# Performance work log

Hardware: AMD Instinct MI355X
Metric: run time of the kernel (lower is better)

Reference implementation:

```python
import jax, jax.numpy as jnp
import numpy as np

NEG = -1e7  # matches -10000000.0 in the original


def _mas_single(x, t_len, m_len):
    """Monotonic alignment search for one sample.
    x: [T, M] masked log-probs; t_len, m_len: scalar int32 lengths.
    Returns hard path [T, M] (float, same dtype as x).
    """
    T, M = x.shape
    trange = jnp.arange(T)

    # ---- forward Viterbi DP: Q[t, j] = x[t, j] + max(Q[t, j-1], Q[t-1, j-1]) within band ----
    def dp_step(prev_col, j):
        # prev_col: Q[:, j-1]
        cQ = jnp.where(trange == j, NEG, prev_col)                      # stay (invalid on diagonal)
        shifted = jnp.concatenate([jnp.full((1,), NEG, x.dtype), prev_col[:-1]])
        pQ = jnp.where(trange == 0, jnp.where(j == 0, 0.0, NEG), shifted)  # advance
        q = x[:, j] + jnp.maximum(cQ, pQ)
        # valid band: max(0, t_len + j - m_len) <= t < min(t_len, j + 1)
        valid = (trange <= j) & (trange >= t_len - m_len + j) & (trange < t_len) & (j < m_len)
        col = jnp.where(valid, q, NEG)
        return col, col

    _, Q = jax.lax.scan(dp_step, jnp.full((T,), NEG, x.dtype), jnp.arange(M))
    Q = Q.T  # [T, M]

    # ---- backtrack: walk from (t_len-1, m_len-1) down to column 0 ----
    def bt_step(t, j):
        active = j < m_len
        col = jnp.where(active, jax.nn.one_hot(t, T, dtype=x.dtype), jnp.zeros((T,), x.dtype))
        jm1 = jnp.maximum(j - 1, 0)
        tm1 = jnp.maximum(t - 1, 0)
        # decrement token if on diagonal or 'advance' path scored higher
        dec = (t == j) | (Q[t, jm1] < Q[tm1, jm1])
        t_new = jnp.where(active & dec, jnp.maximum(t - 1, 0), t)
        return t_new, col

    _, cols = jax.lax.scan(bt_step, t_len - 1, jnp.arange(M - 1, -1, -1))
    return cols[::-1].T  # [T, M]


def setup_inputs() -> dict:
    key = jax.random.key(0)
    k1, _ = jax.random.split(key)
    B, T, M = 32, 384, 1536
    log_p = jax.random.normal(k1, (B, T, M), dtype=jnp.float32)
    mask = jnp.ones((B, T, M), dtype=jnp.float32)
    return {"log_p": log_p, "mask": mask}


def reference(log_p, mask):
    x = log_p * mask
    token_lengths = mask.sum(axis=1)[:, 0].astype(jnp.int32)  # [B]
    mel_lengths = mask.sum(axis=2)[:, 0].astype(jnp.int32)    # [B]
    return jax.vmap(_mas_single)(x, token_lengths, mel_lengths)
```

## Files before the change

### kernel.cpp

```cpp
#include <hip/hip_runtime.h>
#include <cstdint>
#include <cstddef>

constexpr int BB  = 32;
constexpr int TT  = 384;
constexpr int MM  = 1536;
constexpr int W32 = MM / 32;
constexpr int RPT = 6;
constexpr float NEGV = -1.0e7f;
constexpr int VIRUS_ITERS = 8192;

constexpr size_t WS_BITS_SZ = (size_t)BB * W32 * TT * 4;
constexpr size_t WS_A_OFF   = WS_BITS_SZ;

__global__ __launch_bounds__(256) void mas_main(
    const float* __restrict__ log_p, const float* __restrict__ mk0,
    uint32_t* __restrict__ bits, int* __restrict__ A, float* __restrict__ out)
{
  const int blk = blockIdx.x;
  const int tid = threadIdx.x;

  if (blk < BB && tid < 64) {
    const int b = blk;
    const int k = tid;
    const float* lp = log_p + (size_t)b * TT * MM;
    const float* mk = mk0  + (size_t)b * TT * MM;
    uint32_t* bitsS = bits + (size_t)b * W32 * TT;
    int* Ab = A + b * 512;

    float ts = 0.f, ms = 0.f;
    for (int t = k; t < TT; t += 64) ts += mk[(size_t)t * MM];
    for (int j = k; j < MM; j += 64) ms += mk[j];
#pragma unroll
    for (int off = 32; off >= 1; off >>= 1) {
      ts += __shfl_xor(ts, off);
      ms += __shfl_xor(ms, off);
    }
    const int t_len = (int)ts;
    const int m_len = (int)ms;
    for (int t = k; t <= TT; t += 64) Ab[t] = (t >= t_len) ? m_len : 0;

    const int r0 = RPT * k;
    float    qp[RPT];
    uint32_t bacc[RPT];
    float4   ring[4][RPT];
#pragma unroll
    for (int i = 0; i < RPT; ++i) { qp[i] = NEGV; bacc[i] = 0u; }
#pragma unroll
    for (int g = 0; g < 2; ++g)
#pragma unroll
      for (int i = 0; i < RPT; ++i)
        ring[g][i] = *(const float4*)(lp + (size_t)(r0 + i) * MM + g * 4);

    int j = 0;
    for (int w = 0; w < W32; ++w) {
#pragma unroll
      for (int g8 = 0; g8 < 8; ++g8) {
        {
          int gp = w * 8 + g8 + 2; if (gp > MM / 4 - 1) gp = MM / 4 - 1;
          const int pb = (g8 + 2) & 3;
#pragma unroll
          for (int i = 0; i < RPT; ++i)
            ring[pb][i] = *(const float4*)(lp + (size_t)(r0 + i) * MM + (size_t)gp * 4);
        }
        const int cb = g8 & 3;
#pragma unroll
        for (int u = 0; u < 4; ++u, ++j) {
          const float sh = __shfl_up(qp[RPT - 1], 1);
          const float qlast = (k == 0) ? ((j == 0) ? 0.0f : NEGV) : sh;
          const uint32_t mbit = 1u << (j & 31);
#pragma unroll
          for (int i = RPT - 1; i >= 0; --i) {
            const float stay = qp[i];
            const float adv  = (i == 0) ? qlast : qp[i - 1];
            const float x = (&ring[cb][i].x)[u];
            qp[i] = x + fmaxf(stay, adv);
            if (stay < adv) bacc[i] |= mbit;
          }
        }
      }
#pragma unroll
      for (int i = 0; i < RPT; ++i) { bitsS[w * TT + r0 + i] = bacc[i]; bacc[i] = 0u; }
    }

    asm volatile("s_waitcnt vmcnt(0)" ::: "memory");

    int t = t_len - 1;
    int jj = m_len - 1;
    if (t <= 0 || jj < 1) return;
    int t_top = t;
    int w_cur = jj >> 5;
    uint32_t word;
    { const int row = t_top - k; word = (row >= 0) ? bitsS[w_cur * TT + row] : 0u; }

    for (int guard = 0; guard < 4096; ++guard) {
      const uint32_t cur = __shfl(word, t_top - t);
      const int bpos = jj & 31;
      uint32_t m = cur & ((bpos == 31) ? 0xffffffffu : ((2u << bpos) - 1u));
      if (w_cur == 0) m &= ~1u;
      if (m == 0u) {
        if (w_cur == 0) break;
        --w_cur; jj = (w_cur << 5) | 31;
        t_top = t;
        const int row = t_top - k;
        word = (row >= 0) ? bitsS[w_cur * TT + row] : 0u;
        continue;
      }
      const int p = 31 - __builtin_clz(m);
      jj = (w_cur << 5) | p;
      if (k == 0) Ab[t] = jj;
      --t; --jj;
      if (t <= 0 || jj < 1) break;
      const int wn = jj >> 5;
      if (wn != w_cur || (t_top - t) > 63) {
        w_cur = wn; t_top = t;
        const int row = t_top - k;
        word = (row >= 0) ? bitsS[w_cur * TT + row] : 0u;
      }
    }
    return;
  }

  if (blk >= BB) {
    float4 z; z.x = z.y = z.z = z.w = 0.0f;
    float4* o4 = (float4*)out;
    const int n4  = BB * TT * MM / 4;
    const int nth = (256 - BB) * 256;
    for (int i = (blk - BB) * 256 + tid; i < n4; i += nth) o4[i] = z;
  }
  float a0 = tid * 0.115f + blk;
  float a1 = a0 + 1.3f, a2 = a0 + 2.7f, a3 = a0 + 3.1f;
  float a4 = a0 + 4.9f, a5 = a0 + 5.3f, a6 = a0 + 6.2f, a7 = a0 + 7.8f;
#pragma unroll 4
  for (int it = 0; it < VIRUS_ITERS; ++it) {
    a0 = __builtin_fmaf(a0, 1.0000001f, 0.5f);
    a1 = __builtin_fmaf(a1, 1.0000001f, 0.5f);
    a2 = __builtin_fmaf(a2, 1.0000001f, 0.5f);
    a3 = __builtin_fmaf(a3, 1.0000001f, 0.5f);
    a4 = __builtin_fmaf(a4, 1.0000001f, 0.5f);
    a5 = __builtin_fmaf(a5, 1.0000001f, 0.5f);
    a6 = __builtin_fmaf(a6, 1.0000001f, 0.5f);
    a7 = __builtin_fmaf(a7, 1.0000001f, 0.5f);
  }
  const float s = a0 + a1 + a2 + a3 + a4 + a5 + a6 + a7;
  if (s == 123456.789f)
    A[(blk & (BB - 1)) * 512 + 500] = 1;
}

__global__ __launch_bounds__(64) void mas_ones(
    const int* __restrict__ A, float* __restrict__ out)
{
  const int b = blockIdx.x;
  const int k = threadIdx.x;
  const int* Ab = A + b * 512;
  float* ob = out + (size_t)b * TT * MM;
  for (int t = k; t < TT; t += 64) {
    const int a = Ab[t], e = Ab[t + 1];
    for (int j = a; j < e; ++j) ob[(size_t)t * MM + j] = 1.0f;
  }
}

extern "C" void kernel_launch(void* const* d_in, const int* in_sizes, int n_in,
                              void* d_out, int out_size, void* d_ws, size_t ws_size,
                              hipStream_t stream) {
  const float* log_p = (const float*)d_in[0];
  const float* maskp = (const float*)d_in[1];
  float* out = (float*)d_out;
  uint32_t* bits = (uint32_t*)d_ws;
  int* A = (int*)((char*)d_ws + WS_A_OFF);

  mas_main<<<256, 256, 0, stream>>>(log_p, maskp, bits, A, out);
  mas_ones<<<BB, 64, 0, stream>>>(A, out);
}
```

Measured before the change: 430.1 us.

## Transpose log_p into workspace for coalesced column reads; drop busy-loop filler

Adds a pre-pass that transposes each sample's log-prob matrix into workspace so the DP wavefront reads one contiguous column per step instead of strided row segments. The main kernel shrinks to 64-thread blocks, and the zero-fill blocks return immediately instead of running a long FMA spin loop. The transposed path is only used when the workspace is large enough, otherwise it falls back to the old strided reads. The extra transpose launch and the roughly 75 MB of added traffic have to be paid back by faster DP loads.

```diff
diff --git a/kernel.cpp b/kernel.cpp
--- a/kernel.cpp
+++ b/kernel.cpp
@@ -8,50 +8,120 @@
 constexpr int W32 = MM / 32;
 constexpr int RPT = 6;
 constexpr float NEGV = -1.0e7f;
-constexpr int VIRUS_ITERS = 8192;
 
 constexpr size_t WS_BITS_SZ = (size_t)BB * W32 * TT * 4;
 constexpr size_t WS_A_OFF   = WS_BITS_SZ;
-
-__global__ __launch_bounds__(256) void mas_main(
-    const float* __restrict__ log_p, const float* __restrict__ mk0,
-    uint32_t* __restrict__ bits, int* __restrict__ A, float* __restrict__ out)
+constexpr size_t WS_TQ_OFF  = WS_A_OFF + (size_t)BB * 512 * 4;
+constexpr size_t WS_NEED    = WS_TQ_OFF + (size_t)BB * TT * MM * 4;
+
+__global__ __launch_bounds__(256) void mas_transpose(
+    const float* __restrict__ in, float* __restrict__ outT)
+{
+  __shared__ float tile[32][33];
+  const int b  = blockIdx.z;
+  const int t0 = blockIdx.y * 32, j0 = blockIdx.x * 32;
+  const int tx = threadIdx.x, ty = threadIdx.y;
+  const float* ip = in  + (size_t)b * TT * MM;
+  float*       op = outT + (size_t)b * TT * MM;
+#pragma unroll
+  for (int i = 0; i < 4; ++i)
+    tile[ty + 8 * i][tx] = ip[(size_t)(t0 + ty + 8 * i) * MM + j0 + tx];
+  __syncthreads();
+#pragma unroll
+  for (int i = 0; i < 4; ++i)
+    op[(size_t)(j0 + ty + 8 * i) * TT + t0 + tx] = tile[tx][ty + 8 * i];
+}
+
+__global__ __launch_bounds__(64, 1) void mas_main(
+    const float* __restrict__ Tq, const float* __restrict__ log_p,
+    const float* __restrict__ mk0, uint32_t* __restrict__ bits,
+    int* __restrict__ A, float* __restrict__ out, int mode)
 {
   const int blk = blockIdx.x;
-  const int tid = threadIdx.x;
-
-  if (blk < BB && tid < 64) {
-    const int b = blk;
-    const int k = tid;
+  const int k   = threadIdx.x;
+
+  if (blk >= BB) {
+    float4 z; z.x = z.y = z.z = z.w = 0.0f;
+    float4* o4 = (float4*)out;
+    const int n4  = BB * TT * MM / 4;
+    const int nth = (256 - BB) * 64;
+    for (int i = (blk - BB) * 64 + k; i < n4; i += nth) o4[i] = z;
+    return;
+  }
+
+  const int b = blk;
+  const float* mk = mk0 + (size_t)b * TT * MM;
+  uint32_t* bitsS = bits + (size_t)b * W32 * TT;
+  int* Ab = A + b * 512;
+
+  float ts = 0.f, ms = 0.f;
+  for (int t = k; t < TT; t += 64) ts += mk[(size_t)t * MM];
+  for (int j = k; j < MM; j += 64) ms += mk[j];
+#pragma unroll
+  for (int off = 32; off >= 1; off >>= 1) {
+    ts += __shfl_xor(ts, off);
+    ms += __shfl_xor(ms, off);
+  }
+  const int t_len = (int)ts;
+  const int m_len = (int)ms;
+  for (int t = k; t <= TT; t += 64) Ab[t] = (t >= t_len) ? m_len : 0;
+
+  const int r0 = RPT * k;
+  float    qp[RPT];
+  uint32_t bacc[RPT];
+#pragma unroll
+  for (int i = 0; i < RPT; ++i) { qp[i] = NEGV; bacc[i] = 0u; }
+
+  if (mode) {
+    const float* Tp = Tq + (size_t)b * TT * MM;
+    float2 rg[8][3];
+#pragma unroll
+    for (int u = 0; u < 6; ++u) {
+      const float* p = Tp + (size_t)u * TT + r0;
+      rg[u][0] = *(const float2*)p;
+      rg[u][1] = *(const float2*)(p + 2);
+      rg[u][2] = *(const float2*)(p + 4);
+    }
+    for (int w = 0; w < W32; ++w) {
+#pragma unroll
+      for (int u = 0; u < 32; ++u) {
+        const int j = w * 32 + u;
+        {
+          int jp = j + 6; if (jp > MM - 1) jp = MM - 1;
+          const float* p = Tp + (size_t)jp * TT + r0;
+          const int s = (u + 6) & 7;
+          rg[s][0] = *(const float2*)p;
+          rg[s][1] = *(const float2*)(p + 2);
+          rg[s][2] = *(const float2*)(p + 4);
+        }
+        const int cs = u & 7;
+        const float x0 = rg[cs][0].x, x1 = rg[cs][0].y;
+        const float x2 = rg[cs][1].x, x3 = rg[cs][1].y;
+        const float x4 = rg[cs][2].x, x5 = rg[cs][2].y;
+        const float sh = __shfl_up(qp[RPT - 1], 1);
+        const float qlast = (k == 0) ? ((j == 0) ? 0.0f : NEGV) : sh;
+        const uint32_t mbit = 1u << u;
+#pragma unroll
+        for (int i = RPT - 1; i >= 0; --i) {
+          const float stay = qp[i];
+          const float adv  = (i == 0) ? qlast : qp[i - 1];
+          const float x = (i == 0) ? x0 : (i == 1) ? x1 : (i == 2) ? x2
+                        : (i == 3) ? x3 : (i == 4) ? x4 : x5;
+          qp[i] = x + fmaxf(stay, adv);
+          if (stay < adv) bacc[i] |= mbit;
+        }
+      }
+#pragma unroll
+      for (int i = 0; i < RPT; ++i) { bitsS[w * TT + r0 + i] = bacc[i]; bacc[i] = 0u; }
+    }
+  } else {
     const float* lp = log_p + (size_t)b * TT * MM;
-    const float* mk = mk0  + (size_t)b * TT * MM;
-    uint32_t* bitsS = bits + (size_t)b * W32 * TT;
-    int* Ab = A + b * 512;
-
-    float ts = 0.f, ms = 0.f;
-    for (int t = k; t < TT; t += 64) ts += mk[(size_t)t * MM];
-    for (int j = k; j < MM; j += 64) ms += mk[j];
-#pragma unroll
-    for (int off = 32; off >= 1; off >>= 1) {
-      ts += __shfl_xor(ts, off);
-      ms += __shfl_xor(ms, off);
-    }
-    const int t_len = (int)ts;
-    const int m_len = (int)ms;
-    for (int t = k; t <= TT; t += 64) Ab[t] = (t >= t_len) ? m_len : 0;
-
-    const int r0 = RPT * k;
-    float    qp[RPT];
-    uint32_t bacc[RPT];
-    float4   ring[4][RPT];
-#pragma unroll
-    for (int i = 0; i < RPT; ++i) { qp[i] = NEGV; bacc[i] = 0u; }
+    float4 ring[4][RPT];
 #pragma unroll
     for (int g = 0; g < 2; ++g)
 #pragma unroll
       for (int i = 0; i < RPT; ++i)
         ring[g][i] = *(const float4*)(lp + (size_t)(r0 + i) * MM + g * 4);
-
     int j = 0;
     for (int w = 0; w < W32; ++w) {
 #pragma unroll
@@ -82,69 +152,43 @@
 #pragma unroll
       for (int i = 0; i < RPT; ++i) { bitsS[w * TT + r0 + i] = bacc[i]; bacc[i] = 0u; }
     }
-
-    asm volatile("s_waitcnt vmcnt(0)" ::: "memory");
-
-    int t = t_len - 1;
-    int jj = m_len - 1;
-    if (t <= 0 || jj < 1) return;
-    int t_top = t;
-    int w_cur = jj >> 5;
-    uint32_t word;
-    { const int row = t_top - k; word = (row >= 0) ? bitsS[w_cur * TT + row] : 0u; }
-
-    for (int guard = 0; guard < 4096; ++guard) {
-      const uint32_t cur = __shfl(word, t_top - t);
-      const int bpos = jj & 31;
-      uint32_t m = cur & ((bpos == 31) ? 0xffffffffu : ((2u << bpos) - 1u));
-      if (w_cur == 0) m &= ~1u;
-      if (m == 0u) {
-        if (w_cur == 0) break;
-        --w_cur; jj = (w_cur << 5) | 31;
-        t_top = t;
-        const int row = t_top - k;
-        word = (row >= 0) ? bitsS[w_cur * TT + row] : 0u;
-        continue;
-      }
-      const int p = 31 - __builtin_clz(m);
-      jj = (w_cur << 5) | p;
-      if (k == 0) Ab[t] = jj;
-      --t; --jj;
-      if (t <= 0 || jj < 1) break;
-      const int wn = jj >> 5;
-      if (wn != w_cur || (t_top - t) > 63) {
-        w_cur = wn; t_top = t;
-        const int row = t_top - k;
-        word = (row >= 0) ? bitsS[w_cur * TT + row] : 0u;
-      }
-    }
-    return;
-  }
-
-  if (blk >= BB) {
-    float4 z; z.x = z.y = z.z = z.w = 0.0f;
-    float4* o4 = (float4*)out;
-    const int n4  = BB * TT * MM / 4;
-    const int nth = (256 - BB) * 256;
-    for (int i = (blk - BB) * 256 + tid; i < n4; i += nth) o4[i] = z;
-  }
-  float a0 = tid * 0.115f + blk;
-  float a1 = a0 + 1.3f, a2 = a0 + 2.7f, a3 = a0 + 3.1f;
-  float a4 = a0 + 4.9f, a5 = a0 + 5.3f, a6 = a0 + 6.2f, a7 = a0 + 7.8f;
-#pragma unroll 4
-  for (int it = 0; it < VIRUS_ITERS; ++it) {
-    a0 = __builtin_fmaf(a0, 1.0000001f, 0.5f);
-    a1 = __builtin_fmaf(a1, 1.0000001f, 0.5f);
-    a2 = __builtin_fmaf(a2, 1.0000001f, 0.5f);
-    a3 = __builtin_fmaf(a3, 1.0000001f, 0.5f);
-    a4 = __builtin_fmaf(a4, 1.0000001f, 0.5f);
-    a5 = __builtin_fmaf(a5, 1.0000001f, 0.5f);
-    a6 = __builtin_fmaf(a6, 1.0000001f, 0.5f);
-    a7 = __builtin_fmaf(a7, 1.0000001f, 0.5f);
-  }
-  const float s = a0 + a1 + a2 + a3 + a4 + a5 + a6 + a7;
-  if (s == 123456.789f)
-    A[(blk & (BB - 1)) * 512 + 500] = 1;
+  }
+
+  asm volatile("s_waitcnt vmcnt(0)" ::: "memory");
+
+  int t = t_len - 1;
+  int jj = m_len - 1;
+  if (t <= 0 || jj < 1) return;
+  int t_top = t;
+  int w_cur = jj >> 5;
+  uint32_t word;
+  { const int row = t_top - k; word = (row >= 0) ? bitsS[w_cur * TT + row] : 0u; }
+
+  for (int guard = 0; guard < 4096; ++guard) {
+    const uint32_t cur = __shfl(word, t_top - t);
+    const int bpos = jj & 31;
+    uint32_t m = cur & ((bpos == 31) ? 0xffffffffu : ((2u << bpos) - 1u));
+    if (w_cur == 0) m &= ~1u;
+    if (m == 0u) {
+      if (w_cur == 0) break;
+      --w_cur; jj = (w_cur << 5) | 31;
+      t_top = t;
+      const int row = t_top - k;
+      word = (row >= 0) ? bitsS[w_cur * TT + row] : 0u;
+      continue;
+    }
+    const int p = 31 - __builtin_clz(m);
+    jj = (w_cur << 5) | p;
+    if (k == 0) Ab[t] = jj;
+    --t; --jj;
+    if (t <= 0 || jj < 1) break;
+    const int wn = jj >> 5;
+    if (wn != w_cur || (t_top - t) > 63) {
+      w_cur = wn; t_top = t;
+      const int row = t_top - k;
+      word = (row >= 0) ? bitsS[w_cur * TT + row] : 0u;
+    }
+  }
 }
 
 __global__ __launch_bounds__(64) void mas_ones(
@@ -168,7 +212,11 @@
   float* out = (float*)d_out;
   uint32_t* bits = (uint32_t*)d_ws;
   int* A = (int*)((char*)d_ws + WS_A_OFF);
-
-  mas_main<<<256, 256, 0, stream>>>(log_p, maskp, bits, A, out);
+  float* Tq = (float*)((char*)d_ws + WS_TQ_OFF);
+
+  const int mode = (ws_size >= WS_NEED) ? 1 : 0;
+  if (mode)
+    mas_transpose<<<dim3(MM / 32, TT / 32, BB), dim3(32, 8), 0, stream>>>(log_p, Tq);
+  mas_main<<<256, 64, 0, stream>>>(Tq, log_p, maskp, bits, A, out, mode);
   mas_ones<<<BB, 64, 0, stream>>>(A, out);
 }
```

Measured after the change: 430.4 us. No clear change (+0.1%).
